# Performance work log

Hardware: AMD Instinct MI355X
Metric: run time of the kernel (lower is better)

## Reference

```python
import jax, jax.numpy as jnp
import numpy as np

B, T, V, NH, HD = 2, 64, 32000, 32, 32  # head_dim == n_head required by the original einsum
C = NH * HD

def setup_inputs() -> dict:
    key = jax.random.key(0)
    k0, k1, k2 = jax.random.split(key, 3)
    return {
        "x": jax.random.normal(k0, (B, T, C), jnp.float32),
        "W_ffn": jax.random.normal(k1, (HD, HD), jnp.float32) / np.sqrt(HD),
        "b_ffn": jnp.zeros((HD,), jnp.float32),
        "temps": jnp.ones((NH,), jnp.float32),
        "vocab_emb": jax.random.normal(k2, (V, C), jnp.float32) * 0.02,
    }

def reference(x, W_ffn, b_ffn, temps, vocab_emb):
    b, t, c = x.shape
    nh = temps.shape[0]
    hd = c // nh
    v = vocab_emb.shape[0]
    # per-head channel FFN: Linear(head_dim, head_dim) with bias -> x @ W^T + b
    xc = x.reshape(b * t, nh, hd)
    ffn = jnp.einsum('bnh,dh->bnd', xc, W_ffn) + b_ffn  # (BT, nh, hd)
    # vocab channels: (nh, V, hd)
    vocab_ch = vocab_emb.reshape(v, nh, hd).transpose(1, 0, 2)
    # Original torch einsum 'bnh,hvd->bnv' contracts ffn's head_dim axis with
    # vocab_ch's n_head axis (equal sizes) AND sums over d. Mathematically this
    # equals contracting against vocab_sum[h, v] = sum_d vocab_ch[h, v, d].
    vocab_sum = vocab_ch.sum(-1)  # (nh==hd, V)
    logits = jnp.einsum('bnh,hv->bnv', ffn, vocab_sum)  # (BT, nh, V)
    temps_c = jnp.clip(temps, 0.1)[None, :, None]
    weights = jax.nn.softmax(logits / temps_c, axis=-1)
    # Original 'bnv,hvd->bnh' likewise sums d: out[b,n,h] = sum_v w[b,n,v]*vocab_sum[h,v]
    out = jnp.einsum('bnv,hv->bnh', weights, vocab_sum)  # (BT, nh, hd)
    return out.reshape(b, t, c)
```

## Files before the change

### kernel.cpp

```cpp
#include <hip/hip_runtime.h>
#include <hip/hip_bf16.h>

#define NV      32000
#define MROWS   4096
#define NSLICE  8
#define CHUNKS_PER_SLICE 125
#define PART_STRIDE 1056

typedef __attribute__((ext_vector_type(8))) short short8;
typedef __attribute__((ext_vector_type(16))) float f32x16;

#define OFF_VSB  0
#define OFF_VSTB 2048000
#define OFF_FB   4096000
#define OFF_PART 4358144

#define NVS_BLOCKS 1000
#define NF_BLOCKS  512

static __device__ __forceinline__ unsigned pkbf(float lo, float hi) {
    union { __hip_bfloat162 h; unsigned u; } cv;
    cv.h.x = __float2bfloat16(lo);
    cv.h.y = __float2bfloat16(hi);
    return cv.u;
}

__global__ __launch_bounds__(256)
void prep_kernel(const float* __restrict__ emb,
                 const float* __restrict__ x, const float* __restrict__ W,
                 const float* __restrict__ bias, const float* __restrict__ temps,
                 unsigned short* __restrict__ vsb,
                 unsigned short* __restrict__ vstb,
                 unsigned short* __restrict__ Fb) {
    const int blk = blockIdx.x;
    const int tid = threadIdx.x;
    if (blk < NVS_BLOCKS) {
        const int vbase = blk * 32;
        const int wave = tid >> 6, lane = tid & 63;
        __shared__ float lds[32][33];
        for (int vl = wave; vl < 32; vl += 4) {
            const float4* p = (const float4*)(emb + (size_t)(vbase + vl) * 1024) + lane;
            float4 a0 = p[0], a1 = p[64], a2 = p[128], a3 = p[192];
            float s0 = a0.x + a0.y + a0.z + a0.w;
            float s1 = a1.x + a1.y + a1.z + a1.w;
            float s2 = a2.x + a2.y + a2.z + a2.w;
            float s3 = a3.x + a3.y + a3.z + a3.w;
            s0 += __shfl_xor(s0, 1, 64); s0 += __shfl_xor(s0, 2, 64); s0 += __shfl_xor(s0, 4, 64);
            s1 += __shfl_xor(s1, 1, 64); s1 += __shfl_xor(s1, 2, 64); s1 += __shfl_xor(s1, 4, 64);
            s2 += __shfl_xor(s2, 1, 64); s2 += __shfl_xor(s2, 2, 64); s2 += __shfl_xor(s2, 4, 64);
            s3 += __shfl_xor(s3, 1, 64); s3 += __shfl_xor(s3, 2, 64); s3 += __shfl_xor(s3, 4, 64);
            if ((lane & 7) == 0) {
                int hb = lane >> 3;
                lds[vl][hb]      = s0;
                lds[vl][hb + 8]  = s1;
                lds[vl][hb + 16] = s2;
                lds[vl][hb + 24] = s3;
            }
        }
        __syncthreads();
        {
            int v = tid >> 3, h = (tid & 7) * 4;
            union { unsigned u[2]; ushort2 s2[2]; } o;
            o.u[0] = pkbf(lds[v][h],     lds[v][h + 1]);
            o.u[1] = pkbf(lds[v][h + 2], lds[v][h + 3]);
            *(uint2*)(vsb + (size_t)(vbase + v) * 32 + h) = *(uint2*)o.u;
        }
        {
            int h = tid >> 3, vi = (tid & 7) * 4;
            union { unsigned u[2]; } o;
            o.u[0] = pkbf(lds[vi][h],     lds[vi + 1][h]);
            o.u[1] = pkbf(lds[vi + 2][h], lds[vi + 3][h]);
            *(uint2*)(vstb + (size_t)h * NV + vbase + vi) = *(uint2*)o.u;
        }
    } else {
        int t = (blk - NVS_BLOCKS) * 256 + tid;
        int frow = t >> 5, d = t & 31;
        const float4* xp = (const float4*)(x + (size_t)frow * 32);
        const float4* wp = (const float4*)(W + (size_t)d * 32);
        float s = bias[d];
#pragma unroll
        for (int i = 0; i < 8; ++i) {
            float4 xv = xp[i];
            float4 wv = wp[i];
            s += xv.x * wv.x + xv.y * wv.y + xv.z * wv.z + xv.w * wv.w;
        }
        float sc = 1.44269504088896f / fmaxf(temps[frow & 31], 0.1f);
        __hip_bfloat16 bv = __float2bfloat16(s * sc);
        Fb[t] = *reinterpret_cast<unsigned short*>(&bv);
    }
}

__global__ __launch_bounds__(256, 2)
void fused_mfma(const unsigned short* __restrict__ vsb,
                const unsigned short* __restrict__ vstb,
                const unsigned short* __restrict__ Fb,
                float* __restrict__ part) {
    const int b = blockIdx.x;
    const int s = b & 7;
    const int qp = b >> 3;
    const int tid = threadIdx.x;
    const int wave = tid >> 6, lane = tid & 63;
    const int hi = lane >> 5, c = lane & 31;

    const int qrow0 = qp * 64 + c;
    short8 q0a = *(const short8*)(Fb + (size_t)qrow0 * 32 + 8 * hi);
    short8 q0b = *(const short8*)(Fb + (size_t)qrow0 * 32 + 16 + 8 * hi);
    short8 q1a = *(const short8*)(Fb + (size_t)(qrow0 + 32) * 32 + 8 * hi);
    short8 q1b = *(const short8*)(Fb + (size_t)(qrow0 + 32) * 32 + 16 + 8 * hi);

    union { unsigned u[4]; short8 v8; } onesb;
    onesb.u[0] = 0x3F803F80u; onesb.u[1] = 0x3F803F80u;
    onesb.u[2] = 0x3F803F80u; onesb.u[3] = 0x3F803F80u;

    f32x16 oacc0, oacc1, lacc0, lacc1;
#pragma unroll
    for (int r = 0; r < 16; ++r) { oacc0[r] = 0.f; oacc1[r] = 0.f; lacc0[r] = 0.f; lacc1[r] = 0.f; }

    for (int ch = s * CHUNKS_PER_SLICE + wave; ch < (s + 1) * CHUNKS_PER_SLICE; ch += 4) {
        const int vbase = ch * 32;
        const unsigned short* vrow = vsb + (size_t)(vbase + c) * 32 + 8 * hi;
        short8 va0 = *(const short8*)(vrow);
        short8 va1 = *(const short8*)(vrow + 16);
        const unsigned short* vtrow = vstb + (size_t)c * NV + vbase + 8 * hi;
        short8 vb0 = *(const short8*)(vtrow);
        short8 vb1 = *(const short8*)(vtrow + 16);

#pragma unroll
        for (int t = 0; t < 2; ++t) {
            f32x16 sa;
#pragma unroll
            for (int r = 0; r < 16; ++r) sa[r] = 0.f;
            sa = __builtin_amdgcn_mfma_f32_32x32x16_bf16(va0, t ? q1a : q0a, sa, 0, 0, 0);
            sa = __builtin_amdgcn_mfma_f32_32x32x16_bf16(va1, t ? q1b : q0b, sa, 0, 0, 0);

            float w[16];
#pragma unroll
            for (int r = 0; r < 16; ++r) w[r] = __builtin_amdgcn_exp2f(sa[r]);

            unsigned u0 = pkbf(w[0], w[1]),   u1 = pkbf(w[2], w[3]);
            unsigned u2 = pkbf(w[4], w[5]),   u3 = pkbf(w[6], w[7]);
            unsigned u4 = pkbf(w[8], w[9]),   u5 = pkbf(w[10], w[11]);
            unsigned u6 = pkbf(w[12], w[13]), u7 = pkbf(w[14], w[15]);
            asm volatile("v_permlane32_swap_b32 %0, %1" : "+v"(u0), "+v"(u2));
            asm volatile("v_permlane32_swap_b32 %0, %1" : "+v"(u1), "+v"(u3));
            asm volatile("v_permlane32_swap_b32 %0, %1" : "+v"(u4), "+v"(u6));
            asm volatile("v_permlane32_swap_b32 %0, %1" : "+v"(u5), "+v"(u7));

            union { unsigned u[4]; short8 v8; } pa0, pa1;
            pa0.u[0] = u0; pa0.u[1] = u1; pa0.u[2] = u2; pa0.u[3] = u3;
            pa1.u[0] = u4; pa1.u[1] = u5; pa1.u[2] = u6; pa1.u[3] = u7;

            if (t == 0) {
                oacc0 = __builtin_amdgcn_mfma_f32_32x32x16_bf16(pa0.v8, vb0, oacc0, 0, 0, 0);
                oacc0 = __builtin_amdgcn_mfma_f32_32x32x16_bf16(pa1.v8, vb1, oacc0, 0, 0, 0);
                lacc0 = __builtin_amdgcn_mfma_f32_32x32x16_bf16(pa0.v8, onesb.v8, lacc0, 0, 0, 0);
                lacc0 = __builtin_amdgcn_mfma_f32_32x32x16_bf16(pa1.v8, onesb.v8, lacc0, 0, 0, 0);
            } else {
                oacc1 = __builtin_amdgcn_mfma_f32_32x32x16_bf16(pa0.v8, vb0, oacc1, 0, 0, 0);
                oacc1 = __builtin_amdgcn_mfma_f32_32x32x16_bf16(pa1.v8, vb1, oacc1, 0, 0, 0);
                lacc1 = __builtin_amdgcn_mfma_f32_32x32x16_bf16(pa0.v8, onesb.v8, lacc1, 0, 0, 0);
                lacc1 = __builtin_amdgcn_mfma_f32_32x32x16_bf16(pa1.v8, onesb.v8, lacc1, 0, 0, 0);
            }
        }
    }

    __shared__ float red[2][4][64 * 17];
    __shared__ float lred[2][4][32];
    {
        float* rw0 = &red[0][wave][lane * 17];
        float* rw1 = &red[1][wave][lane * 17];
#pragma unroll
        for (int r = 0; r < 16; ++r) { rw0[r] = oacc0[r]; rw1[r] = oacc1[r]; }
        if (c == 0) {
#pragma unroll
            for (int r = 0; r < 16; ++r) {
                int q = (r & 3) + 8 * (r >> 2) + 4 * hi;
                lred[0][wave][q] = lacc0[r];
                lred[1][wave][q] = lacc1[r];
            }
        }
    }
    __syncthreads();

#pragma unroll
    for (int t = 0; t < 2; ++t) {
        const size_t pbase = (size_t)((qp * 2 + t) * NSLICE + s) * PART_STRIDE;
        for (int idx = tid; idx < 1024; idx += 256) {
            int ln = idx >> 4, r = idx & 15;
            float sum = red[t][0][ln * 17 + r] + red[t][1][ln * 17 + r]
                      + red[t][2][ln * 17 + r] + red[t][3][ln * 17 + r];
            int lhi = ln >> 5, lc = ln & 31;
            int q = (r & 3) + 8 * (r >> 2) + 4 * lhi;
            part[pbase + (q << 5) + lc] = sum;
        }
        if (tid < 32)
            part[pbase + 1024 + tid] = lred[t][0][tid] + lred[t][1][tid]
                                     + lred[t][2][tid] + lred[t][3][tid];
    }
}

__global__ void combine_kernel(const float* __restrict__ part, float* __restrict__ out) {
    int t = blockIdx.x * 256 + threadIdx.x;
    if (t >= MROWS * 32) return;
    int qrow = t >> 5, j = t & 31;
    int qt = qrow >> 5, qi = qrow & 31;
    float a = 0.f, l = 0.f;
#pragma unroll
    for (int s = 0; s < NSLICE; ++s) {
        const float* p = part + (size_t)(qt * NSLICE + s) * PART_STRIDE;
        a += p[(qi << 5) + j];
        l += p[1024 + qi];
    }
    out[t] = a / l;
}

extern "C" void kernel_launch(void* const* d_in, const int* in_sizes, int n_in,
                              void* d_out, int out_size, void* d_ws, size_t ws_size,
                              hipStream_t stream) {
    const float* x     = (const float*)d_in[0];
    const float* W     = (const float*)d_in[1];
    const float* bias  = (const float*)d_in[2];
    const float* temps = (const float*)d_in[3];
    const float* emb   = (const float*)d_in[4];
    float* out = (float*)d_out;

    char* ws = (char*)d_ws;
    unsigned short* vsb  = (unsigned short*)(ws + OFF_VSB);
    unsigned short* vstb = (unsigned short*)(ws + OFF_VSTB);
    unsigned short* Fb   = (unsigned short*)(ws + OFF_FB);
    float*          part = (float*)(ws + OFF_PART);

    prep_kernel<<<NVS_BLOCKS + NF_BLOCKS, 256, 0, stream>>>(emb, x, W, bias, temps,
                                                            vsb, vstb, Fb);
    fused_mfma<<<64 * NSLICE, 256, 0, stream>>>(vsb, vstb, Fb, part);
    combine_kernel<<<(MROWS * 32 + 255) / 256, 256, 0, stream>>>(part, out);
}
```

Baseline: 60.75 us.

## Fuse combine into MFMA kernel via last-block counter, prefetch chunks, nontemporal emb loads

Removes the separate combine kernel launch by having the last slice block for each query pair, detected with an atomic counter reset in the prep kernel, perform the cross-slice reduction and write the output. The main loop is software-pipelined with double-buffered register loads so the next chunk's vsb/vstb data is fetched while the current chunk computes. Embedding loads in prep become nontemporal. Costs include extra registers for the prefetch buffers, threadfence/atomic synchronisation, and a serialized tail in the last-arriving blocks.

```diff
diff --git a/kernel.cpp b/kernel.cpp
--- a/kernel.cpp
+++ b/kernel.cpp
@@ -9,11 +9,13 @@
 
 typedef __attribute__((ext_vector_type(8))) short short8;
 typedef __attribute__((ext_vector_type(16))) float f32x16;
+typedef __attribute__((ext_vector_type(4))) float f32x4;
 
 #define OFF_VSB  0
 #define OFF_VSTB 2048000
 #define OFF_FB   4096000
 #define OFF_PART 4358144
+#define OFF_CNT  8683520
 
 #define NVS_BLOCKS 1000
 #define NF_BLOCKS  512
@@ -23,6 +25,9 @@
     cv.h.x = __float2bfloat16(lo);
     cv.h.y = __float2bfloat16(hi);
     return cv.u;
+}
+static __device__ __forceinline__ f32x4 ntload(const float* p) {
+    return __builtin_nontemporal_load((const f32x4*)p);
 }
 
 __global__ __launch_bounds__(256)
@@ -31,16 +36,18 @@
                  const float* __restrict__ bias, const float* __restrict__ temps,
                  unsigned short* __restrict__ vsb,
                  unsigned short* __restrict__ vstb,
-                 unsigned short* __restrict__ Fb) {
+                 unsigned short* __restrict__ Fb,
+                 int* __restrict__ cnt) {
     const int blk = blockIdx.x;
     const int tid = threadIdx.x;
+    if (blk == 0 && tid < 64) cnt[tid] = 0;
     if (blk < NVS_BLOCKS) {
         const int vbase = blk * 32;
         const int wave = tid >> 6, lane = tid & 63;
         __shared__ float lds[32][33];
         for (int vl = wave; vl < 32; vl += 4) {
-            const float4* p = (const float4*)(emb + (size_t)(vbase + vl) * 1024) + lane;
-            float4 a0 = p[0], a1 = p[64], a2 = p[128], a3 = p[192];
+            const float* p = emb + (size_t)(vbase + vl) * 1024 + lane * 4;
+            f32x4 a0 = ntload(p), a1 = ntload(p + 256), a2 = ntload(p + 512), a3 = ntload(p + 768);
             float s0 = a0.x + a0.y + a0.z + a0.w;
             float s1 = a1.x + a1.y + a1.z + a1.w;
             float s2 = a2.x + a2.y + a2.z + a2.w;
@@ -60,17 +67,17 @@
         __syncthreads();
         {
             int v = tid >> 3, h = (tid & 7) * 4;
-            union { unsigned u[2]; ushort2 s2[2]; } o;
-            o.u[0] = pkbf(lds[v][h],     lds[v][h + 1]);
-            o.u[1] = pkbf(lds[v][h + 2], lds[v][h + 3]);
-            *(uint2*)(vsb + (size_t)(vbase + v) * 32 + h) = *(uint2*)o.u;
+            unsigned o[2];
+            o[0] = pkbf(lds[v][h],     lds[v][h + 1]);
+            o[1] = pkbf(lds[v][h + 2], lds[v][h + 3]);
+            *(uint2*)(vsb + (size_t)(vbase + v) * 32 + h) = *(uint2*)o;
         }
         {
             int h = tid >> 3, vi = (tid & 7) * 4;
-            union { unsigned u[2]; } o;
-            o.u[0] = pkbf(lds[vi][h],     lds[vi + 1][h]);
-            o.u[1] = pkbf(lds[vi + 2][h], lds[vi + 3][h]);
-            *(uint2*)(vstb + (size_t)h * NV + vbase + vi) = *(uint2*)o.u;
+            unsigned o[2];
+            o[0] = pkbf(lds[vi][h],     lds[vi + 1][h]);
+            o[1] = pkbf(lds[vi + 2][h], lds[vi + 3][h]);
+            *(uint2*)(vstb + (size_t)h * NV + vbase + vi) = *(uint2*)o;
         }
     } else {
         int t = (blk - NVS_BLOCKS) * 256 + tid;
@@ -90,11 +97,50 @@
     }
 }
 
+
+#define LOADCH(VA0, VA1, VB0, VB1, CH) do {                                        \
+    const unsigned short* _vr = vsb + ((size_t)(CH) << 10) + (c << 5) + (hi << 3); \
+    VA0 = *(const short8*)(_vr);                                                   \
+    VA1 = *(const short8*)(_vr + 16);                                              \
+    const unsigned short* _vt = vstb + (size_t)c * NV + ((CH) << 5) + (hi << 3);   \
+    VB0 = *(const short8*)(_vt);                                                   \
+    VB1 = *(const short8*)(_vt + 16);                                              \
+} while (0)
+
+#define TILE(QA, QB, OACC, LACC, VA0, VA1, VB0, VB1) do {                          \
+    f32x16 sa = __builtin_amdgcn_mfma_f32_32x32x16_bf16(VA0, QA, fz, 0, 0, 0);     \
+    sa = __builtin_amdgcn_mfma_f32_32x32x16_bf16(VA1, QB, sa, 0, 0, 0);            \
+    float w[16];                                                                   \
+    _Pragma("unroll")                                                              \
+    for (int r = 0; r < 16; ++r) w[r] = __builtin_amdgcn_exp2f(sa[r]);             \
+    unsigned u0 = pkbf(w[0], w[1]),   u1 = pkbf(w[2], w[3]);                       \
+    unsigned u2 = pkbf(w[4], w[5]),   u3 = pkbf(w[6], w[7]);                       \
+    unsigned u4 = pkbf(w[8], w[9]),   u5 = pkbf(w[10], w[11]);                     \
+    unsigned u6 = pkbf(w[12], w[13]), u7 = pkbf(w[14], w[15]);                     \
+    asm volatile("v_permlane32_swap_b32 %0, %1" : "+v"(u0), "+v"(u2));             \
+    asm volatile("v_permlane32_swap_b32 %0, %1" : "+v"(u1), "+v"(u3));             \
+    asm volatile("v_permlane32_swap_b32 %0, %1" : "+v"(u4), "+v"(u6));             \
+    asm volatile("v_permlane32_swap_b32 %0, %1" : "+v"(u5), "+v"(u7));             \
+    union { unsigned u[4]; short8 v8; } pa0, pa1;                                  \
+    pa0.u[0] = u0; pa0.u[1] = u1; pa0.u[2] = u2; pa0.u[3] = u3;                    \
+    pa1.u[0] = u4; pa1.u[1] = u5; pa1.u[2] = u6; pa1.u[3] = u7;                    \
+    OACC = __builtin_amdgcn_mfma_f32_32x32x16_bf16(pa0.v8, VB0, OACC, 0, 0, 0);    \
+    OACC = __builtin_amdgcn_mfma_f32_32x32x16_bf16(pa1.v8, VB1, OACC, 0, 0, 0);    \
+    LACC = __builtin_amdgcn_mfma_f32_32x32x16_bf16(pa0.v8, onesv, LACC, 0, 0, 0);  \
+    LACC = __builtin_amdgcn_mfma_f32_32x32x16_bf16(pa1.v8, onesv, LACC, 0, 0, 0);  \
+} while (0)
+
+#define COMPUTE(VA0, VA1, VB0, VB1) do {                                           \
+    TILE(q0a, q0b, oacc0, lacc0, VA0, VA1, VB0, VB1);                              \
+    TILE(q1a, q1b, oacc1, lacc1, VA0, VA1, VB0, VB1);                              \
+} while (0)
+
 __global__ __launch_bounds__(256, 2)
 void fused_mfma(const unsigned short* __restrict__ vsb,
                 const unsigned short* __restrict__ vstb,
                 const unsigned short* __restrict__ Fb,
-                float* __restrict__ part) {
+                float* __restrict__ part, int* __restrict__ cnt,
+                float* __restrict__ out) {
     const int b = blockIdx.x;
     const int s = b & 7;
     const int qp = b >> 3;
@@ -108,60 +154,33 @@
     short8 q1a = *(const short8*)(Fb + (size_t)(qrow0 + 32) * 32 + 8 * hi);
     short8 q1b = *(const short8*)(Fb + (size_t)(qrow0 + 32) * 32 + 16 + 8 * hi);
 
-    union { unsigned u[4]; short8 v8; } onesb;
-    onesb.u[0] = 0x3F803F80u; onesb.u[1] = 0x3F803F80u;
-    onesb.u[2] = 0x3F803F80u; onesb.u[3] = 0x3F803F80u;
-
-    f32x16 oacc0, oacc1, lacc0, lacc1;
-#pragma unroll
-    for (int r = 0; r < 16; ++r) { oacc0[r] = 0.f; oacc1[r] = 0.f; lacc0[r] = 0.f; lacc1[r] = 0.f; }
-
-    for (int ch = s * CHUNKS_PER_SLICE + wave; ch < (s + 1) * CHUNKS_PER_SLICE; ch += 4) {
-        const int vbase = ch * 32;
-        const unsigned short* vrow = vsb + (size_t)(vbase + c) * 32 + 8 * hi;
-        short8 va0 = *(const short8*)(vrow);
-        short8 va1 = *(const short8*)(vrow + 16);
-        const unsigned short* vtrow = vstb + (size_t)c * NV + vbase + 8 * hi;
-        short8 vb0 = *(const short8*)(vtrow);
-        short8 vb1 = *(const short8*)(vtrow + 16);
-
-#pragma unroll
-        for (int t = 0; t < 2; ++t) {
-            f32x16 sa;
-#pragma unroll
-            for (int r = 0; r < 16; ++r) sa[r] = 0.f;
-            sa = __builtin_amdgcn_mfma_f32_32x32x16_bf16(va0, t ? q1a : q0a, sa, 0, 0, 0);
-            sa = __builtin_amdgcn_mfma_f32_32x32x16_bf16(va1, t ? q1b : q0b, sa, 0, 0, 0);
-
-            float w[16];
-#pragma unroll
-            for (int r = 0; r < 16; ++r) w[r] = __builtin_amdgcn_exp2f(sa[r]);
-
-            unsigned u0 = pkbf(w[0], w[1]),   u1 = pkbf(w[2], w[3]);
-            unsigned u2 = pkbf(w[4], w[5]),   u3 = pkbf(w[6], w[7]);
-            unsigned u4 = pkbf(w[8], w[9]),   u5 = pkbf(w[10], w[11]);
-            unsigned u6 = pkbf(w[12], w[13]), u7 = pkbf(w[14], w[15]);
-            asm volatile("v_permlane32_swap_b32 %0, %1" : "+v"(u0), "+v"(u2));
-            asm volatile("v_permlane32_swap_b32 %0, %1" : "+v"(u1), "+v"(u3));
-            asm volatile("v_permlane32_swap_b32 %0, %1" : "+v"(u4), "+v"(u6));
-            asm volatile("v_permlane32_swap_b32 %0, %1" : "+v"(u5), "+v"(u7));
-
-            union { unsigned u[4]; short8 v8; } pa0, pa1;
-            pa0.u[0] = u0; pa0.u[1] = u1; pa0.u[2] = u2; pa0.u[3] = u3;
-            pa1.u[0] = u4; pa1.u[1] = u5; pa1.u[2] = u6; pa1.u[3] = u7;
-
-            if (t == 0) {
-                oacc0 = __builtin_amdgcn_mfma_f32_32x32x16_bf16(pa0.v8, vb0, oacc0, 0, 0, 0);
-                oacc0 = __builtin_amdgcn_mfma_f32_32x32x16_bf16(pa1.v8, vb1, oacc0, 0, 0, 0);
-                lacc0 = __builtin_amdgcn_mfma_f32_32x32x16_bf16(pa0.v8, onesb.v8, lacc0, 0, 0, 0);
-                lacc0 = __builtin_amdgcn_mfma_f32_32x32x16_bf16(pa1.v8, onesb.v8, lacc0, 0, 0, 0);
-            } else {
-                oacc1 = __builtin_amdgcn_mfma_f32_32x32x16_bf16(pa0.v8, vb0, oacc1, 0, 0, 0);
-                oacc1 = __builtin_amdgcn_mfma_f32_32x32x16_bf16(pa1.v8, vb1, oacc1, 0, 0, 0);
-                lacc1 = __builtin_amdgcn_mfma_f32_32x32x16_bf16(pa0.v8, onesb.v8, lacc1, 0, 0, 0);
-                lacc1 = __builtin_amdgcn_mfma_f32_32x32x16_bf16(pa1.v8, onesb.v8, lacc1, 0, 0, 0);
-            }
-        }
+    union { unsigned u[4]; short8 v8; } onesu;
+    onesu.u[0] = 0x3F803F80u; onesu.u[1] = 0x3F803F80u;
+    onesu.u[2] = 0x3F803F80u; onesu.u[3] = 0x3F803F80u;
+    const short8 onesv = onesu.v8;
+
+    f32x16 fz, oacc0, oacc1, lacc0, lacc1;
+#pragma unroll
+    for (int r = 0; r < 16; ++r) { fz[r] = 0.f; oacc0[r] = 0.f; oacc1[r] = 0.f; lacc0[r] = 0.f; lacc1[r] = 0.f; }
+
+    const int n = (CHUNKS_PER_SLICE - wave + 3) >> 2;
+    int ch = s * CHUNKS_PER_SLICE + wave;
+    short8 a0, a1, a2, a3, b0, b1, b2, b3;
+    LOADCH(a0, a1, a2, a3, ch);
+    int i = 1;
+    for (; i + 1 < n; i += 2) {
+        LOADCH(b0, b1, b2, b3, ch + 4);
+        COMPUTE(a0, a1, a2, a3);
+        LOADCH(a0, a1, a2, a3, ch + 8);
+        COMPUTE(b0, b1, b2, b3);
+        ch += 8;
+    }
+    if (i < n) {
+        LOADCH(b0, b1, b2, b3, ch + 4);
+        COMPUTE(a0, a1, a2, a3);
+        COMPUTE(b0, b1, b2, b3);
+    } else {
+        COMPUTE(a0, a1, a2, a3);
     }
 
     __shared__ float red[2][4][64 * 17];
@@ -197,21 +216,27 @@
             part[pbase + 1024 + tid] = lred[t][0][tid] + lred[t][1][tid]
                                      + lred[t][2][tid] + lred[t][3][tid];
     }
-}
-
-__global__ void combine_kernel(const float* __restrict__ part, float* __restrict__ out) {
-    int t = blockIdx.x * 256 + threadIdx.x;
-    if (t >= MROWS * 32) return;
-    int qrow = t >> 5, j = t & 31;
-    int qt = qrow >> 5, qi = qrow & 31;
-    float a = 0.f, l = 0.f;
-#pragma unroll
-    for (int s = 0; s < NSLICE; ++s) {
-        const float* p = part + (size_t)(qt * NSLICE + s) * PART_STRIDE;
-        a += p[(qi << 5) + j];
-        l += p[1024 + qi];
-    }
-    out[t] = a / l;
+
+    __threadfence();
+    __syncthreads();
+    __shared__ int sdone;
+    if (tid == 0) sdone = (atomicAdd(&cnt[qp], 1) == NSLICE - 1) ? 1 : 0;
+    __syncthreads();
+    if (sdone) {
+        __threadfence();
+        for (int t2 = tid; t2 < 2048; t2 += 256) {
+            int lr = t2 >> 5, j = t2 & 31;
+            int qt = qp * 2 + (lr >> 5), qi = lr & 31;
+            float a = 0.f, l = 0.f;
+#pragma unroll
+            for (int sl = 0; sl < NSLICE; ++sl) {
+                const float* p = part + (size_t)(qt * NSLICE + sl) * PART_STRIDE;
+                a += p[(qi << 5) + j];
+                l += p[1024 + qi];
+            }
+            out[(size_t)qp * 2048 + t2] = a / l;
+        }
+    }
 }
 
 extern "C" void kernel_launch(void* const* d_in, const int* in_sizes, int n_in,
@@ -229,9 +254,9 @@
     unsigned short* vstb = (unsigned short*)(ws + OFF_VSTB);
     unsigned short* Fb   = (unsigned short*)(ws + OFF_FB);
     float*          part = (float*)(ws + OFF_PART);
+    int*            cnt  = (int*)(ws + OFF_CNT);
 
     prep_kernel<<<NVS_BLOCKS + NF_BLOCKS, 256, 0, stream>>>(emb, x, W, bias, temps,
-                                                            vsb, vstb, Fb);
-    fused_mfma<<<64 * NSLICE, 256, 0, stream>>>(vsb, vstb, Fb, part);
-    combine_kernel<<<(MROWS * 32 + 255) / 256, 256, 0, stream>>>(part, out);
-}
+                                                            vsb, vstb, Fb, cnt);
+    fused_mfma<<<64 * NSLICE, 256, 0, stream>>>(vsb, vstb, Fb, part, cnt, out);
+}
```

Result: slower. 146.7 us (+141.4%).
